# Kernel optimization log

Measured on AMD Instinct MI355X. Metric: run time of the kernel, lower is better.

## Reference

```python
import jax, jax.numpy as jnp
import numpy as np

N_NODES = 100000


def _gcn_conv(h, src, dst, W, b, n_nodes):
    """PyG GCNConv with add_self_loops=True, symmetric normalization.
    out = D^-1/2 (A + I) D^-1/2 (h W) + b, aggregating src->dst."""
    h = h @ W  # transform first (out_dim <= in_dim), as PyG does
    ones = jnp.ones(src.shape[0], dtype=h.dtype)
    deg = jax.ops.segment_sum(ones, dst, num_segments=n_nodes) + 1.0  # +1 self loop
    dinv = jax.lax.rsqrt(deg)
    coef = dinv[src] * dinv[dst]  # per-edge norm
    agg = jax.ops.segment_sum(h[src] * coef[:, None], dst, num_segments=n_nodes)
    agg = agg + h * (dinv * dinv)[:, None]  # self-loop term: dinv_i^2 * h_i
    return agg + b


def setup_inputs() -> dict:
    key = jax.random.key(0)
    k1, k2, k3, k4 = jax.random.split(key, 4)
    x = jax.random.normal(k1, (N_NODES, 256), dtype=jnp.float32)
    edge_index = jax.random.randint(k2, (2, 1600000), 0, N_NODES, dtype=jnp.int64)
    W1 = jax.random.normal(k3, (256, 128), dtype=jnp.float32) * (1.0 / np.sqrt(256))
    b1 = jnp.zeros((128,), dtype=jnp.float32)
    W2 = jax.random.normal(k4, (128, 64), dtype=jnp.float32) * (1.0 / np.sqrt(128))
    b2 = jnp.zeros((64,), dtype=jnp.float32)
    return {"x": x, "edge_index": edge_index, "W1": W1, "b1": b1, "W2": W2, "b2": b2}


def reference(x, edge_index, W1, b1, W2, b2):
    src, dst = edge_index[0], edge_index[1]
    h = jax.nn.relu(_gcn_conv(x, src, dst, W1, b1, N_NODES))
    # dropout is identity in eval mode
    h = _gcn_conv(h, src, dst, W2, b2, N_NODES)
    return jax.nn.log_softmax(h, axis=1)
```

## Files before the change

### kernel.cpp

```cpp
#include <hip/hip_runtime.h>
#include <hip/hip_bf16.h>


#define N_NODES 100000
#define F_IN 256
#define F_MID 128
#define F_OUT 64

#define BSHIFT 8
#define BNODES 256
#define NBUCKETS ((N_NODES + BNODES - 1) / BNODES)
#define BCAP 6144
#define EPB 4096

typedef __attribute__((ext_vector_type(8))) short short8;
typedef __attribute__((ext_vector_type(4))) float f32x4;

__device__ inline ushort bf16_rne(float f) {
    uint u = __float_as_uint(f);
    u += 0x7FFF + ((u >> 16) & 1);
    return (ushort)(u >> 16);
}
__device__ inline float lo16(uint r) { return __uint_as_float(r << 16); }
__device__ inline float hi16(uint r) { return __uint_as_float(r & 0xffff0000u); }
__device__ inline uint pack_bf2(float a, float b) {
    return (uint)bf16_rne(a) | ((uint)bf16_rne(b) << 16);
}


__global__ __launch_bounds__(256)
void bucket_scatter_kernel(const int* __restrict__ src, const int* __restrict__ dst,
                           int* __restrict__ bcur, uint* __restrict__ ebuf, int E) {
    __shared__ int hist[512], ps[512], cur[512];
    __shared__ int base[NBUCKETS];
    __shared__ uint   eLoc[EPB];
    __shared__ ushort bLoc[EPB];
    int t = threadIdx.x;
    int e0 = blockIdx.x * EPB;
    int e1 = e0 + EPB; if (e1 > E) e1 = E;
    int ne = e1 - e0;

    for (int i = t; i < 512; i += 256) hist[i] = 0;
    __syncthreads();
    for (int i = t; i < ne; i += 256) atomicAdd(&hist[dst[e0 + i] >> BSHIFT], 1);
    __syncthreads();
    ps[t] = hist[t]; ps[t + 256] = hist[t + 256];
    __syncthreads();
#pragma unroll
    for (int off = 1; off < 512; off <<= 1) {
        int i0 = t, i1 = t + 256;
        int v0 = (i0 >= off) ? ps[i0 - off] : 0;
        int v1 = (i1 >= off) ? ps[i1 - off] : 0;
        __syncthreads();
        ps[i0] += v0; ps[i1] += v1;
        __syncthreads();
    }
    {
        int ex0 = ps[t] - hist[t];
        int ex1 = ps[t + 256] - hist[t + 256];
        __syncthreads();
        ps[t] = ex0; ps[t + 256] = ex1;
        cur[t] = ex0; cur[t + 256] = ex1;
    }
    __syncthreads();
    for (int i = t; i < ne; i += 256) {
        int d = dst[e0 + i], s = src[e0 + i];
        int b = d >> BSHIFT;
        int p = atomicAdd(&cur[b], 1);
        eLoc[p] = ((uint)(d & (BNODES - 1)) << 17) | (uint)s;
        bLoc[p] = (ushort)b;
    }
    __syncthreads();
    for (int b = t; b < NBUCKETS; b += 256) {
        int h = hist[b];
        base[b] = h ? atomicAdd(&bcur[b], h) : 0;
    }
    __syncthreads();
    for (int i = t; i < ne; i += 256) {
        int b = bLoc[i];
        int d = base[b] + (i - ps[b]);
        if (d < BCAP) ebuf[(size_t)b * BCAP + d] = eLoc[i];
    }
}

__global__ __launch_bounds__(256)
void bucket_sort_kernel(const uint* __restrict__ ebuf, const int* __restrict__ bcur,
                        int* __restrict__ ssrc, int* __restrict__ rs, int* __restrict__ cnt,
                        float* __restrict__ dinv, int n) {
    __shared__ uint eL[BCAP];
    __shared__ int  sLoc[BCAP];
    __shared__ int hist[BNODES], ps[BNODES];
    int b = blockIdx.x, t = threadIdx.x;
    int nb = bcur[b];
    if (nb > BCAP) nb = BCAP;
    for (int i = t; i < nb; i += 256) eL[i] = ebuf[(size_t)b * BCAP + i];
    hist[t] = 0;
    __syncthreads();
    for (int i = t; i < nb; i += 256) atomicAdd(&hist[eL[i] >> 17], 1);
    __syncthreads();
    ps[t] = hist[t];
    __syncthreads();
#pragma unroll
    for (int off = 1; off < BNODES; off <<= 1) {
        int v = (t >= off) ? ps[t - off] : 0;
        __syncthreads();
        ps[t] += v;
        __syncthreads();
    }
    int excl = ps[t] - hist[t];
    int node = b * BNODES + t;
    if (node < n) {
        rs[node] = b * BCAP + excl;
        cnt[node] = hist[t];
        dinv[node] = 1.0f / sqrtf((float)hist[t] + 1.0f);
    }
    __syncthreads();
    ps[t] = excl;
    __syncthreads();
    for (int i = t; i < nb; i += 256) {
        uint e = eL[i];
        int d = e >> 17;
        int p = atomicAdd(&ps[d], 1);
        sLoc[p] = (int)(e & 0x1FFFF);
    }
    __syncthreads();
    for (int i = t; i < nb; i += 256) ssrc[(size_t)b * BCAP + i] = sLoc[i];
}

__global__ __launch_bounds__(256)
void wprep_kernel(const float* __restrict__ W1, const float* __restrict__ W2,
                  short8* __restrict__ W1f, short8* __restrict__ W2f) {
    int b = blockIdx.x;
    if (b < 16) {
        int f = b * 256 + threadIdx.x;
        int k0 = f >> 9, nt = (f >> 6) & 7, ln = f & 63;
        int kbase = k0 * 32 + (ln >> 4) * 8;
        int n = nt * 16 + (ln & 15);
        short8 fr;
#pragma unroll
        for (int j = 0; j < 8; ++j) fr[j] = (short)bf16_rne(W1[(kbase + j) * F_MID + n]);
        W1f[f] = fr;
    } else {
        int f = (b - 16) * 256 + threadIdx.x;
        int k0 = f >> 8, nt = (f >> 6) & 3, ln = f & 63;
        int kbase = k0 * 32 + (ln >> 4) * 8;
        int n = nt * 16 + (ln & 15);
        short8 fr;
#pragma unroll
        for (int j = 0; j < 8; ++j) fr[j] = (short)bf16_rne(W2[(kbase + j) * F_OUT + n]);
        W2f[f] = fr;
    }
}


__global__ __launch_bounds__(512, 2)
void gemm1_kernel(const float* __restrict__ A, const short8* __restrict__ Wf,
                  const float* __restrict__ dinv, ushort* __restrict__ C,
                  int M) {
    __shared__ short8 BsF[4096];
    __shared__ ushort Abuf[2][128 * 64];
    int tid = threadIdx.x;
    int lane = tid & 63, w = tid >> 6;
    int m0 = blockIdx.x * 128;

    int o0 = tid * 2;
    int srow = o0 >> 3;
    int gr = m0 + srow; if (gr >= M) gr = m0;
    int cl0 = o0 & 7, cl1 = cl0 + 1;
    int cg0 = cl0 ^ (srow & 7), cg1 = cl1 ^ (srow & 7);
    const float* arow = &A[(size_t)gr * F_IN];

    float4 rv[2][2];
    rv[0][0] = ((const float4*)(arow + cg0 * 8))[0];
    rv[0][1] = ((const float4*)(arow + cg0 * 8))[1];
    rv[1][0] = ((const float4*)(arow + cg1 * 8))[0];
    rv[1][1] = ((const float4*)(arow + cg1 * 8))[1];

    for (int f = tid; f < 4096; f += 512) BsF[f] = Wf[f];

    {
        short8 pk;
        pk[0] = (short)bf16_rne(rv[0][0].x); pk[1] = (short)bf16_rne(rv[0][0].y);
        pk[2] = (short)bf16_rne(rv[0][0].z); pk[3] = (short)bf16_rne(rv[0][0].w);
        pk[4] = (short)bf16_rne(rv[0][1].x); pk[5] = (short)bf16_rne(rv[0][1].y);
        pk[6] = (short)bf16_rne(rv[0][1].z); pk[7] = (short)bf16_rne(rv[0][1].w);
        *(short8*)&Abuf[0][o0 * 8] = pk;
        pk[0] = (short)bf16_rne(rv[1][0].x); pk[1] = (short)bf16_rne(rv[1][0].y);
        pk[2] = (short)bf16_rne(rv[1][0].z); pk[3] = (short)bf16_rne(rv[1][0].w);
        pk[4] = (short)bf16_rne(rv[1][1].x); pk[5] = (short)bf16_rne(rv[1][1].y);
        pk[6] = (short)bf16_rne(rv[1][1].z); pk[7] = (short)bf16_rne(rv[1][1].w);
        *(short8*)&Abuf[0][(o0 + 1) * 8] = pk;
    }
    __syncthreads();

    f32x4 acc[8];
#pragma unroll
    for (int nt = 0; nt < 8; ++nt) acc[nt] = (f32x4){0.f, 0.f, 0.f, 0.f};

    int arow16 = w * 16 + (lane & 15);
    int asw = arow16 & 7;
    int abase = arow16 * 8;

#pragma unroll
    for (int kc = 0; kc < 4; ++kc) {
        int b = kc & 1;
        if (kc < 3) {
            const float* s0 = arow + (kc + 1) * 64 + cg0 * 8;
            const float* s1 = arow + (kc + 1) * 64 + cg1 * 8;
            rv[0][0] = ((const float4*)s0)[0];
            rv[0][1] = ((const float4*)s0)[1];
            rv[1][0] = ((const float4*)s1)[0];
            rv[1][1] = ((const float4*)s1)[1];
            asm volatile("" ::: "memory");
        }
#pragma unroll
        for (int kk = 0; kk < 2; ++kk) {
            int k0 = kc * 2 + kk;
            int c = kk * 4 + (lane >> 4);
            short8 af = *(const short8*)&Abuf[b][(abase + (c ^ asw)) * 8];
#pragma unroll
            for (int nt = 0; nt < 8; ++nt) {
                short8 bfr = BsF[(k0 * 8 + nt) * 64 + lane];
                acc[nt] = __builtin_amdgcn_mfma_f32_16x16x32_bf16(af, bfr, acc[nt], 0, 0, 0);
            }
        }
        if (kc < 3) {
            short8 pk;
            pk[0] = (short)bf16_rne(rv[0][0].x); pk[1] = (short)bf16_rne(rv[0][0].y);
            pk[2] = (short)bf16_rne(rv[0][0].z); pk[3] = (short)bf16_rne(rv[0][0].w);
            pk[4] = (short)bf16_rne(rv[0][1].x); pk[5] = (short)bf16_rne(rv[0][1].y);
            pk[6] = (short)bf16_rne(rv[0][1].z); pk[7] = (short)bf16_rne(rv[0][1].w);
            *(short8*)&Abuf[b ^ 1][o0 * 8] = pk;
            pk[0] = (short)bf16_rne(rv[1][0].x); pk[1] = (short)bf16_rne(rv[1][0].y);
            pk[2] = (short)bf16_rne(rv[1][0].z); pk[3] = (short)bf16_rne(rv[1][0].w);
            pk[4] = (short)bf16_rne(rv[1][1].x); pk[5] = (short)bf16_rne(rv[1][1].y);
            pk[6] = (short)bf16_rne(rv[1][1].z); pk[7] = (short)bf16_rne(rv[1][1].w);
            *(short8*)&Abuf[b ^ 1][(o0 + 1) * 8] = pk;
        }
        __syncthreads();
    }

#pragma unroll
    for (int i = 0; i < 4; ++i) {
        int r = blockIdx.x * 128 + w * 16 + (lane >> 4) * 4 + i;
        if (r < M) {
            float dv = dinv[r];
#pragma unroll
            for (int nt = 0; nt < 8; ++nt)
                C[(size_t)r * F_MID + nt * 16 + (lane & 15)] = bf16_rne(dv * acc[nt][i]);
        }
    }
}

__global__ __launch_bounds__(256)
void agg1f_kernel(const uint4* __restrict__ h, const int* __restrict__ rs,
                  const int* __restrict__ cnt, const int* __restrict__ ssrc,
                  const float* __restrict__ dinv, const float* __restrict__ bias,
                  const short8* __restrict__ W2f, ushort* __restrict__ h2, int n) {
    __shared__ __align__(16) ushort rowsL[16][136];
    int w = threadIdx.x >> 6, lane = threadIdx.x & 63;
    int q = lane >> 4, c16 = lane & 15;
    int nbase = blockIdx.x * 16;
    const float4* b4 = (const float4*)bias;
    float4 b0 = b4[c16 * 2], b1v = b4[c16 * 2 + 1];

#pragma unroll
    for (int i = 0; i < 4; ++i) {
        int node = nbase + w * 4 + i;
        bool nOk = (node < n);
        int start = nOk ? rs[node] : 0;
        int c = nOk ? cnt[node] : 0;
        float dn = nOk ? dinv[node] : 0.f;
        float a[8];
#pragma unroll
        for (int k = 0; k < 8; ++k) a[k] = 0.f;

        for (int base = 0; base < c; base += 16) {
            bool p[4];
            int s[4];
            uint4 r[4];
#pragma unroll
            for (int j = 0; j < 4; ++j) {
                int e = base + j * 4 + q;
                p[j] = e < c;
                if (p[j]) s[j] = ssrc[start + e];
            }
#pragma unroll
            for (int j = 0; j < 4; ++j)
                if (p[j]) r[j] = h[(size_t)s[j] * 16 + c16];
#pragma unroll
            for (int j = 0; j < 4; ++j) {
                if (p[j]) {
                    a[0] += lo16(r[j].x); a[1] += hi16(r[j].x);
                    a[2] += lo16(r[j].y); a[3] += hi16(r[j].y);
                    a[4] += lo16(r[j].z); a[5] += hi16(r[j].z);
                    a[6] += lo16(r[j].w); a[7] += hi16(r[j].w);
                }
            }
        }
#pragma unroll
        for (int k = 0; k < 8; ++k) {
            a[k] += __shfl_xor(a[k], 16);
            a[k] += __shfl_xor(a[k], 32);
        }
        if (q == 0) {
            short8 pk;
            if (nOk) {
                uint4 sr = h[(size_t)node * 16 + c16];
                float o0 = fmaxf(fmaf(dn, a[0] + lo16(sr.x), b0.x), 0.f);
                float o1 = fmaxf(fmaf(dn, a[1] + hi16(sr.x), b0.y), 0.f);
                float o2 = fmaxf(fmaf(dn, a[2] + lo16(sr.y), b0.z), 0.f);
                float o3 = fmaxf(fmaf(dn, a[3] + hi16(sr.y), b0.w), 0.f);
                float o4 = fmaxf(fmaf(dn, a[4] + lo16(sr.z), b1v.x), 0.f);
                float o5 = fmaxf(fmaf(dn, a[5] + hi16(sr.z), b1v.y), 0.f);
                float o6 = fmaxf(fmaf(dn, a[6] + lo16(sr.w), b1v.z), 0.f);
                float o7 = fmaxf(fmaf(dn, a[7] + hi16(sr.w), b1v.w), 0.f);
                pk[0] = (short)bf16_rne(o0); pk[1] = (short)bf16_rne(o1);
                pk[2] = (short)bf16_rne(o2); pk[3] = (short)bf16_rne(o3);
                pk[4] = (short)bf16_rne(o4); pk[5] = (short)bf16_rne(o5);
                pk[6] = (short)bf16_rne(o6); pk[7] = (short)bf16_rne(o7);
            } else {
                pk = (short8){0, 0, 0, 0, 0, 0, 0, 0};
            }
            *(short8*)&rowsL[w * 4 + i][c16 * 8] = pk;
        }
    }
    __syncthreads();

    f32x4 acc = (f32x4){0.f, 0.f, 0.f, 0.f};
    int ar = lane & 15;
#pragma unroll
    for (int k0 = 0; k0 < 4; ++k0) {
        short8 af = *(const short8*)&rowsL[ar][k0 * 32 + (lane >> 4) * 8];
        short8 bfr = W2f[(k0 * 4 + w) * 64 + lane];
        acc = __builtin_amdgcn_mfma_f32_16x16x32_bf16(af, bfr, acc, 0, 0, 0);
    }
#pragma unroll
    for (int i = 0; i < 4; ++i) {
        int r = (lane >> 4) * 4 + i;
        int node = nbase + r;
        if (node < n) {
            float dv = dinv[node];
            h2[(size_t)node * F_OUT + w * 16 + (lane & 15)] = bf16_rne(dv * acc[i]);
        }
    }
}

__global__ __launch_bounds__(256)
void agg2_kernel(const uint2* __restrict__ h, const int* __restrict__ rs,
                 const int* __restrict__ cnt, const int* __restrict__ ssrc,
                 const float* __restrict__ dinv, const float* __restrict__ bias,
                 float4* __restrict__ out4, int n) {
    int w = threadIdx.x >> 6, lane = threadIdx.x & 63;
    int node = blockIdx.x * 4 + w;
    if (node >= n) return;
    int q = lane >> 4, c16 = lane & 15;
    int start = rs[node], c = cnt[node];
    float dn = dinv[node];
    float a[4];
#pragma unroll
    for (int i = 0; i < 4; ++i) a[i] = 0.f;

    for (int base = 0; base < c; base += 16) {
        bool p[4];
        int s[4];
        uint2 r[4];
#pragma unroll
        for (int j = 0; j < 4; ++j) {
            int e = base + j * 4 + q;
            p[j] = e < c;
            if (p[j]) s[j] = ssrc[start + e];
        }
#pragma unroll
        for (int j = 0; j < 4; ++j)
            if (p[j]) r[j] = h[(size_t)s[j] * 16 + c16];
#pragma unroll
        for (int j = 0; j < 4; ++j) {
            if (p[j]) {
                a[0] += lo16(r[j].x); a[1] += hi16(r[j].x);
                a[2] += lo16(r[j].y); a[3] += hi16(r[j].y);
            }
        }
    }
#pragma unroll
    for (int i = 0; i < 4; ++i) {
        a[i] += __shfl_xor(a[i], 16);
        a[i] += __shfl_xor(a[i], 32);
    }
    uint2 sr = h[(size_t)node * 16 + c16];
    float4 bv = ((const float4*)bias)[c16];
    float v0 = fmaf(dn, a[0] + lo16(sr.x), bv.x);
    float v1 = fmaf(dn, a[1] + hi16(sr.x), bv.y);
    float v2 = fmaf(dn, a[2] + lo16(sr.y), bv.z);
    float v3 = fmaf(dn, a[3] + hi16(sr.y), bv.w);
    float m = fmaxf(fmaxf(v0, v1), fmaxf(v2, v3));
#pragma unroll
    for (int off = 1; off < 16; off <<= 1) m = fmaxf(m, __shfl_xor(m, off));
    float ssum = expf(v0 - m) + expf(v1 - m) + expf(v2 - m) + expf(v3 - m);
#pragma unroll
    for (int off = 1; off < 16; off <<= 1) ssum += __shfl_xor(ssum, off);
    float lg = m + logf(ssum);
    if (q == 0) out4[(size_t)node * 16 + c16] = make_float4(v0 - lg, v1 - lg, v2 - lg, v3 - lg);
}


extern "C" void kernel_launch(void* const* d_in, const int* in_sizes, int n_in,
                              void* d_out, int out_size, void* d_ws, size_t ws_size,
                              hipStream_t stream) {
    const float* x  = (const float*)d_in[0];
    const int*   ei = (const int*)d_in[1];
    const float* W1 = (const float*)d_in[2];
    const float* b1 = (const float*)d_in[3];
    const float* W2 = (const float*)d_in[4];
    const float* b2 = (const float*)d_in[5];
    float* out = (float*)d_out;

    const int N = N_NODES;
    const int E = in_sizes[1] / 2;
    const int* src = ei;
    const int* dst = ei + E;

    char* ws = (char*)d_ws;
    size_t off = 0;
    auto alloc = [&](size_t bytes) {
        char* p = ws + off;
        off = (off + bytes + 255) & ~(size_t)255;
        return p;
    };
    int*    bcur   = (int*)alloc(NBUCKETS * 4);
    int*    rs     = (int*)alloc(N * 4);
    int*    cnt    = (int*)alloc(N * 4);
    float*  dinv   = (float*)alloc(N * 4);
    short8* W1f    = (short8*)alloc(4096 * 16);
    short8* W2f    = (short8*)alloc(1024 * 16);
    uint*   ebuf   = (uint*)alloc((size_t)NBUCKETS * BCAP * 4);
    int*    ssrc   = (int*)alloc((size_t)NBUCKETS * BCAP * 4);
    uint*   h1     = (uint*)alloc((size_t)N * 64 * 4);
    ushort* h2     = (ushort*)alloc((size_t)N * 64 * 2);

    const int nScatBlocks = (E + EPB - 1) / EPB;
    const int nAgg1Blocks = (N + 15) / 16;
    const int nAgg2Blocks = (N + 3) / 4;
    const int nTiles      = (N + 127) / 128;

    hipMemsetAsync(bcur, 0, NBUCKETS * 4, stream);
    wprep_kernel<<<20, 256, 0, stream>>>(W1, W2, W1f, W2f);

    bucket_scatter_kernel<<<nScatBlocks, 256, 0, stream>>>(src, dst, bcur, ebuf, E);
    bucket_sort_kernel<<<NBUCKETS, 256, 0, stream>>>(ebuf, bcur, ssrc, rs, cnt, dinv, N);

    gemm1_kernel<<<nTiles, 512, 0, stream>>>(x, W1f, dinv, (ushort*)h1, N);
    agg1f_kernel<<<nAgg1Blocks, 256, 0, stream>>>((const uint4*)h1, rs, cnt, ssrc, dinv, b1,
                                                  W2f, h2, N);
    agg2_kernel<<<nAgg2Blocks, 256, 0, stream>>>((const uint2*)h2, rs, cnt, ssrc, dinv, b2,
                                                 (float4*)out, N);
}
```

Baseline: 359.3 us.

## Read GEMM1 weights from global memory and process two nodes per wave in agg2

gemm1 no longer stages the 64KB bf16 weight fragments in shared memory. It reads them straight from global memory (through cache) and raises the launch bound to 4 blocks per SM, aiming for higher occupancy and no LDS fill. agg2 now gives each wave two destination nodes and interleaves their gather loads, raising memory-level parallelism and halving the block count. The trade-offs are repeated global or L2 reads of the weights inside the MFMA loop, and some idle lanes when the two nodes have very different degrees.

```diff
diff --git a/kernel.cpp b/kernel.cpp
--- a/kernel.cpp
+++ b/kernel.cpp
@@ -153,11 +153,10 @@
 }
 
 
-__global__ __launch_bounds__(512, 2)
+__global__ __launch_bounds__(512, 4)
 void gemm1_kernel(const float* __restrict__ A, const short8* __restrict__ Wf,
                   const float* __restrict__ dinv, ushort* __restrict__ C,
                   int M) {
-    __shared__ short8 BsF[4096];
     __shared__ ushort Abuf[2][128 * 64];
     int tid = threadIdx.x;
     int lane = tid & 63, w = tid >> 6;
@@ -175,8 +174,6 @@
     rv[0][1] = ((const float4*)(arow + cg0 * 8))[1];
     rv[1][0] = ((const float4*)(arow + cg1 * 8))[0];
     rv[1][1] = ((const float4*)(arow + cg1 * 8))[1];
-
-    for (int f = tid; f < 4096; f += 512) BsF[f] = Wf[f];
 
     {
         short8 pk;
@@ -220,7 +217,7 @@
             short8 af = *(const short8*)&Abuf[b][(abase + (c ^ asw)) * 8];
 #pragma unroll
             for (int nt = 0; nt < 8; ++nt) {
-                short8 bfr = BsF[(k0 * 8 + nt) * 64 + lane];
+                short8 bfr = Wf[(k0 * 8 + nt) * 64 + lane];
                 acc[nt] = __builtin_amdgcn_mfma_f32_16x16x32_bf16(af, bfr, acc[nt], 0, 0, 0);
             }
         }
@@ -352,55 +349,87 @@
                  const float* __restrict__ dinv, const float* __restrict__ bias,
                  float4* __restrict__ out4, int n) {
     int w = threadIdx.x >> 6, lane = threadIdx.x & 63;
-    int node = blockIdx.x * 4 + w;
-    if (node >= n) return;
     int q = lane >> 4, c16 = lane & 15;
-    int start = rs[node], c = cnt[node];
-    float dn = dinv[node];
-    float a[4];
-#pragma unroll
-    for (int i = 0; i < 4; ++i) a[i] = 0.f;
-
-    for (int base = 0; base < c; base += 16) {
-        bool p[4];
-        int s[4];
-        uint2 r[4];
+    int nodeA = blockIdx.x * 8 + w * 2;
+    int nodeB = nodeA + 1;
+    bool okA = (nodeA < n), okB = (nodeB < n);
+    if (!okA) return;
+    int startA = rs[nodeA], cA = cnt[nodeA];
+    int startB = okB ? rs[nodeB] : 0, cB = okB ? cnt[nodeB] : 0;
+    float dnA = dinv[nodeA];
+    float dnB = okB ? dinv[nodeB] : 0.f;
+    float aA[4], aB[4];
+#pragma unroll
+    for (int i = 0; i < 4; ++i) { aA[i] = 0.f; aB[i] = 0.f; }
+
+    int cm = cA > cB ? cA : cB;
+    for (int base = 0; base < cm; base += 16) {
+        bool pA[4], pB[4];
+        int sA[4], sB[4];
+        uint2 rA[4], rB[4];
 #pragma unroll
         for (int j = 0; j < 4; ++j) {
             int e = base + j * 4 + q;
-            p[j] = e < c;
-            if (p[j]) s[j] = ssrc[start + e];
-        }
-#pragma unroll
-        for (int j = 0; j < 4; ++j)
-            if (p[j]) r[j] = h[(size_t)s[j] * 16 + c16];
+            pA[j] = e < cA;
+            pB[j] = e < cB;
+            if (pA[j]) sA[j] = ssrc[startA + e];
+            if (pB[j]) sB[j] = ssrc[startB + e];
+        }
 #pragma unroll
         for (int j = 0; j < 4; ++j) {
-            if (p[j]) {
-                a[0] += lo16(r[j].x); a[1] += hi16(r[j].x);
-                a[2] += lo16(r[j].y); a[3] += hi16(r[j].y);
+            if (pA[j]) rA[j] = h[(size_t)sA[j] * 16 + c16];
+            if (pB[j]) rB[j] = h[(size_t)sB[j] * 16 + c16];
+        }
+#pragma unroll
+        for (int j = 0; j < 4; ++j) {
+            if (pA[j]) {
+                aA[0] += lo16(rA[j].x); aA[1] += hi16(rA[j].x);
+                aA[2] += lo16(rA[j].y); aA[3] += hi16(rA[j].y);
+            }
+            if (pB[j]) {
+                aB[0] += lo16(rB[j].x); aB[1] += hi16(rB[j].x);
+                aB[2] += lo16(rB[j].y); aB[3] += hi16(rB[j].y);
             }
         }
     }
 #pragma unroll
     for (int i = 0; i < 4; ++i) {
-        a[i] += __shfl_xor(a[i], 16);
-        a[i] += __shfl_xor(a[i], 32);
-    }
-    uint2 sr = h[(size_t)node * 16 + c16];
+        aA[i] += __shfl_xor(aA[i], 16);
+        aA[i] += __shfl_xor(aA[i], 32);
+        aB[i] += __shfl_xor(aB[i], 16);
+        aB[i] += __shfl_xor(aB[i], 32);
+    }
     float4 bv = ((const float4*)bias)[c16];
-    float v0 = fmaf(dn, a[0] + lo16(sr.x), bv.x);
-    float v1 = fmaf(dn, a[1] + hi16(sr.x), bv.y);
-    float v2 = fmaf(dn, a[2] + lo16(sr.y), bv.z);
-    float v3 = fmaf(dn, a[3] + hi16(sr.y), bv.w);
-    float m = fmaxf(fmaxf(v0, v1), fmaxf(v2, v3));
-#pragma unroll
-    for (int off = 1; off < 16; off <<= 1) m = fmaxf(m, __shfl_xor(m, off));
-    float ssum = expf(v0 - m) + expf(v1 - m) + expf(v2 - m) + expf(v3 - m);
-#pragma unroll
-    for (int off = 1; off < 16; off <<= 1) ssum += __shfl_xor(ssum, off);
-    float lg = m + logf(ssum);
-    if (q == 0) out4[(size_t)node * 16 + c16] = make_float4(v0 - lg, v1 - lg, v2 - lg, v3 - lg);
+    {
+        uint2 sr = h[(size_t)nodeA * 16 + c16];
+        float v0 = fmaf(dnA, aA[0] + lo16(sr.x), bv.x);
+        float v1 = fmaf(dnA, aA[1] + hi16(sr.x), bv.y);
+        float v2 = fmaf(dnA, aA[2] + lo16(sr.y), bv.z);
+        float v3 = fmaf(dnA, aA[3] + hi16(sr.y), bv.w);
+        float m = fmaxf(fmaxf(v0, v1), fmaxf(v2, v3));
+#pragma unroll
+        for (int off = 1; off < 16; off <<= 1) m = fmaxf(m, __shfl_xor(m, off));
+        float ssum = expf(v0 - m) + expf(v1 - m) + expf(v2 - m) + expf(v3 - m);
+#pragma unroll
+        for (int off = 1; off < 16; off <<= 1) ssum += __shfl_xor(ssum, off);
+        float lg = m + logf(ssum);
+        if (q == 0) out4[(size_t)nodeA * 16 + c16] = make_float4(v0 - lg, v1 - lg, v2 - lg, v3 - lg);
+    }
+    if (okB) {
+        uint2 sr = h[(size_t)nodeB * 16 + c16];
+        float v0 = fmaf(dnB, aB[0] + lo16(sr.x), bv.x);
+        float v1 = fmaf(dnB, aB[1] + hi16(sr.x), bv.y);
+        float v2 = fmaf(dnB, aB[2] + lo16(sr.y), bv.z);
+        float v3 = fmaf(dnB, aB[3] + hi16(sr.y), bv.w);
+        float m = fmaxf(fmaxf(v0, v1), fmaxf(v2, v3));
+#pragma unroll
+        for (int off = 1; off < 16; off <<= 1) m = fmaxf(m, __shfl_xor(m, off));
+        float ssum = expf(v0 - m) + expf(v1 - m) + expf(v2 - m) + expf(v3 - m);
+#pragma unroll
+        for (int off = 1; off < 16; off <<= 1) ssum += __shfl_xor(ssum, off);
+        float lg = m + logf(ssum);
+        if (q == 0) out4[(size_t)nodeB * 16 + c16] = make_float4(v0 - lg, v1 - lg, v2 - lg, v3 - lg);
+    }
 }
 
 
@@ -440,7 +469,7 @@
 
     const int nScatBlocks = (E + EPB - 1) / EPB;
     const int nAgg1Blocks = (N + 15) / 16;
-    const int nAgg2Blocks = (N + 3) / 4;
+    const int nAgg2Blocks = (N + 7) / 8;
     const int nTiles      = (N + 127) / 128;
 
     hipMemsetAsync(bcur, 0, NBUCKETS * 4, stream);
```

After: 352.9 us. Within noise of the previous version (-1.8%).
